# Kernel tuning notes

Hardware: AMD Instinct MI355X
Metric: run time of the kernel (lower is better)

The kernel has to match this reference:

```python
import jax, jax.numpy as jnp
import numpy as np

G, N0, E0 = 10000, 32, 64          # graphs, nodes/graph, edges/graph
NF, NEF, H, D = 64, 64, 128, 256   # num_features, num_edge_features, nhid, ddi_nhid
B = 4096                           # ddi batch_size (pos edges; neg edges follow)
NEG_DECAY = 0.5
RATIO = 0.5


def _lin(k, fan_in, shape):
    s = 1.0 / np.sqrt(fan_in)
    return jax.random.uniform(k, shape, jnp.float32, -s, s)


def setup_inputs() -> dict:
    key = jax.random.key(0)
    ks = jax.random.split(key, 40)
    N, E = G * N0, G * E0
    x = jax.random.normal(ks[0], (N, NF), jnp.float32)
    off = jnp.repeat(jnp.arange(G, dtype=jnp.int32) * N0, E0)
    edge_src = off + jax.random.randint(ks[1], (E,), 0, N0, jnp.int32)
    edge_dst = off + jax.random.randint(ks[2], (E,), 0, N0, jnp.int32)
    edge_weight = jax.random.uniform(ks[3], (E,), jnp.float32)
    ddi_edge_index = jax.random.randint(ks[4], (2, 2 * B), 0, G, jnp.int32)
    ddi_edge_attr = jax.random.normal(ks[5], (2 * B, NEF), jnp.float32)
    p = {}
    p['W1'] = _lin(ks[6], NF, (NF, H)); p['b1'] = jnp.zeros((H,), jnp.float32)
    p['Ws1r'] = _lin(ks[7], H, (H, 1)); p['Ws1n'] = _lin(ks[8], H, (H, 1)); p['bs1'] = jnp.zeros((1,), jnp.float32)
    p['W2'] = _lin(ks[9], H, (H, H)); p['b2'] = jnp.zeros((H,), jnp.float32)
    p['Ws2r'] = _lin(ks[10], H, (H, 1)); p['Ws2n'] = _lin(ks[11], H, (H, 1)); p['bs2'] = jnp.zeros((1,), jnp.float32)
    p['W3'] = _lin(ks[12], H, (H, H)); p['b3'] = jnp.zeros((H,), jnp.float32)
    p['Ws3r'] = _lin(ks[13], H, (H, 1)); p['Ws3n'] = _lin(ks[14], H, (H, 1)); p['bs3'] = jnp.zeros((1,), jnp.float32)
    p['Wd'] = _lin(ks[15], 6 * H, (6 * H, D)); p['bd'] = jnp.zeros((D,), jnp.float32)
    p['Wl1'] = _lin(ks[16], D, (D, D)); p['bl1'] = _lin(ks[17], D, (D,))
    p['Wl2'] = _lin(ks[18], D, (D, D)); p['bl2'] = _lin(ks[19], D, (D,))
    p['Wl3'] = _lin(ks[20], NEF, (NEF, D)); p['bl3'] = _lin(ks[21], NEF, (D,))
    return dict(x=x, edge_src=edge_src, edge_dst=edge_dst, edge_weight=edge_weight,
                ddi_edge_index=ddi_edge_index, ddi_edge_attr=ddi_edge_attr, **p)


def gcn(x, src, dst, ew, W, b):
    # PyG GCNConv: add self-loops (weight 1), symmetric normalization, sum-aggregate
    h = x @ W                                              # [N, out]
    deg = jnp.zeros(x.shape[0], x.dtype).at[dst].add(ew) + 1.0
    dis = jax.lax.rsqrt(deg)
    norm = dis[src] * ew * dis[dst]                        # [E]
    out = jnp.zeros_like(h).at[dst].add(norm[:, None] * h[src])
    out = out + (dis * dis)[:, None] * h                   # self-loop term
    return out + b


def sag_pool(x, src, dst, ew, Wr, Wn, bn, n_per_graph):
    # SAGPooling: score = tanh(GraphConv(x)); keep top ceil(ratio*n) nodes per graph
    N, Hd = x.shape
    g = N // n_per_graph
    agg = jnp.zeros((N, Hd), x.dtype).at[dst].add(ew[:, None] * x[src])
    score = jnp.tanh((agg @ Wn + bn + x @ Wr)[:, 0])       # [N]
    k = int(np.ceil(RATIO * n_per_graph))
    topv, topi = jax.lax.top_k(score.reshape(g, n_per_graph), k)   # [g, k]
    perm = (jnp.arange(g, dtype=jnp.int32)[:, None] * n_per_graph + topi.astype(jnp.int32)).reshape(-1)
    xk = x[perm] * topv.reshape(-1)[:, None]               # gate kept nodes by score
    old2new = jnp.full((N,), -1, jnp.int32).at[perm].set(jnp.arange(g * k, dtype=jnp.int32))
    ns, nd = old2new[src], old2new[dst]
    valid = (ns >= 0) & (nd >= 0)
    new_ew = jnp.where(valid, ew, 0.0)                     # zero-weight == filtered edge
    ns = jnp.where(valid, ns, 0)
    nd = jnp.where(valid, nd, 0)
    return xk, ns, nd, new_ew, k


def readout(x, k):
    # gmp || gap with contiguous, equal-size graphs
    xg = x.reshape(-1, k, x.shape[1])
    return jnp.concatenate([xg.max(axis=1), xg.mean(axis=1)], axis=1)


def reference(x, edge_src, edge_dst, edge_weight, ddi_edge_index, ddi_edge_attr,
              W1, b1, Ws1r, Ws1n, bs1, W2, b2, Ws2r, Ws2n, bs2,
              W3, b3, Ws3r, Ws3n, bs3, Wd, bd, Wl1, bl1, Wl2, bl2, Wl3, bl3):
    h = jax.nn.relu(gcn(x, edge_src, edge_dst, edge_weight, W1, b1))
    h, s, d, ew, k1 = sag_pool(h, edge_src, edge_dst, edge_weight, Ws1r, Ws1n, bs1, N0)
    x1 = readout(h, k1)
    h = jax.nn.relu(gcn(h, s, d, ew, W2, b2))
    h, s, d, ew, k2 = sag_pool(h, s, d, ew, Ws2r, Ws2n, bs2, k1)
    x2 = readout(h, k2)
    h = jax.nn.relu(gcn(h, s, d, ew, W3, b3))
    h, s, d, ew, k3 = sag_pool(h, s, d, ew, Ws3r, Ws3n, bs3, k2)
    x3 = readout(h, k3)
    feat = jnp.concatenate([x1, x2, x3], axis=1)           # [G, 6H] drug features
    # dropout_ratio=0.0 (eval): identity
    ds, dd = ddi_edge_index[0], ddi_edge_index[1]
    dew = jnp.ones(ds.shape, feat.dtype)
    z = jax.nn.relu(gcn(feat, ds, dd, dew, Wd, bd))        # [G, D]
    src_f, tgt_f = z[ds], z[dd]
    pos_x = jax.nn.sigmoid(src_f[:B] @ Wl1 + bl1)
    pos_y = jax.nn.sigmoid(tgt_f[:B] @ Wl2 + bl2)
    neg_x = jax.nn.sigmoid(src_f[B:] @ Wl1 + bl1)
    neg_y = jax.nn.sigmoid(tgt_f[B:] @ Wl2 + bl2)
    pos_a = jax.nn.sigmoid(ddi_edge_attr[:B] @ Wl3 + bl3)
    neg_a = jax.nn.sigmoid(ddi_edge_attr[B:] @ Wl3 + bl3)
    lp = pos_x + pos_a - pos_y
    ln = neg_x + neg_a - neg_y
    norm_pos = jnp.linalg.norm(lp, axis=1)
    norm_neg = jnp.linalg.norm(ln, axis=1)
    loss = 2.0 * D - norm_pos + NEG_DECAY * norm_neg
    return loss, norm_pos, norm_neg, pos_x
```

## Files before the change

### kernel.cpp

```cpp
#include <hip/hip_runtime.h>
#include <math.h>

#define GG   10000
#define NN0  32
#define EE0  64
#define NFF  64
#define HH   128
#define DD   256
#define BB   4096
#define E2B  8192
#define SIXH 768
#define APAD 36

typedef unsigned short u16;
typedef __attribute__((ext_vector_type(8))) short short8v;
typedef __attribute__((ext_vector_type(4))) short short4v;
typedef __attribute__((ext_vector_type(4))) float f32x4;
typedef _Float16 h8f __attribute__((ext_vector_type(8)));
typedef _Float16 h4f __attribute__((ext_vector_type(4)));

static __device__ __forceinline__ u16 f2bf(float x) {
  unsigned u = __float_as_uint(x);
  return (u16)((u + 0x7FFFu + ((u >> 16) & 1u)) >> 16);
}
static __device__ __forceinline__ float bf2f(u16 h) {
  return __uint_as_float(((unsigned)h) << 16);
}


template<int M, int KK, int K, int SX, bool IND, bool LAST>
__device__ __forceinline__ void stage(
    const _Float16* __restrict__ WTh, const _Float16* __restrict__ WTl,
    const float* __restrict__ bg,
    const float* __restrict__ Wr, const float* __restrict__ Wn, const float* __restrict__ bs,
    float* bufX, _Float16* ybh, _Float16* ybl, float* s_A,
    float* s_dis, float* s_cm, float* s_sc2,
    float* s_v1p, float* s_v2p, float* s_score, int* s_rank, int* s_inv,
    int& src_r, int& dst_r, float& ew_r,
    u16* __restrict__ featg, int t)
{
  constexpr int KP = K + 8;
  constexpr int RT  = (M > 16) ? 2 : 1;
  constexpr int CTW = (RT == 2) ? 4 : 2;
  constexpr int KF  = K / 32;
  constexpr int NS  = (RT == 2) ? 2 : 4;

  if (t < EE0)
    atomicAdd(&s_A[dst_r*APAD + src_r], ew_r);
  __syncthreads();

  if (t < M) {
    float deg = 1.f;
#pragma unroll
    for (int m0 = 0; m0 < M; m0 += 4) {
      const float4 a4 = *(const float4*)(s_A + t*APAD + m0);
      deg += a4.x + a4.y + a4.z + a4.w;
    }
    const float dis = rsqrtf(deg);
    const float gg = IND ? s_score[s_inv[t]] : 1.f;
    s_dis[t] = dis; s_cm[t] = dis*gg; s_sc2[t] = dis*dis*gg;
  }
  __syncthreads();

  {
    constexpr int CGB = K/4, RGB = 256/CGB, R = M/RGB;
    const int cg = t % CGB, rg = t / CGB;
    const int c0 = cg * 4;
    float acc[R][4];
#pragma unroll
    for (int i = 0; i < R; ++i) { acc[i][0]=0.f; acc[i][1]=0.f; acc[i][2]=0.f; acc[i][3]=0.f; }
#pragma unroll 2
    for (int m0 = 0; m0 < M; m0 += 4) {
      float4 a[R];
#pragma unroll
      for (int i = 0; i < R; ++i)
        a[i] = *(const float4*)(s_A + (rg*R + i)*APAD + m0);
#pragma unroll
      for (int j = 0; j < 4; ++j) {
        const int m = m0 + j;
        const int row = IND ? s_inv[m] : m;
        const float4 xv = *(const float4*)(bufX + row*SX + c0);
        const float cmm = s_cm[m];
#pragma unroll
        for (int i = 0; i < R; ++i) {
          const float aj = (j==0) ? a[i].x : (j==1) ? a[i].y : (j==2) ? a[i].z : a[i].w;
          const float cf = aj * cmm;
          acc[i][0] = fmaf(cf, xv.x, acc[i][0]);
          acc[i][1] = fmaf(cf, xv.y, acc[i][1]);
          acc[i][2] = fmaf(cf, xv.z, acc[i][2]);
          acc[i][3] = fmaf(cf, xv.w, acc[i][3]);
        }
      }
    }
#pragma unroll
    for (int i = 0; i < R; ++i) {
      const int r = rg*R + i;
      const int rr = IND ? s_inv[r] : r;
      const float4 xv = *(const float4*)(bufX + rr*SX + c0);
      const float dr = s_dis[r], sc = s_sc2[r];
      float4 v;
      v.x = fmaf(sc, xv.x, acc[i][0]*dr);
      v.y = fmaf(sc, xv.y, acc[i][1]*dr);
      v.z = fmaf(sc, xv.z, acc[i][2]*dr);
      v.w = fmaf(sc, xv.w, acc[i][3]*dr);
      h4f vh, vl;
      _Float16 h;
      h = (_Float16)v.x; vh[0] = h; vl[0] = (_Float16)((v.x - (float)h) * 2048.f);
      h = (_Float16)v.y; vh[1] = h; vl[1] = (_Float16)((v.y - (float)h) * 2048.f);
      h = (_Float16)v.z; vh[2] = h; vl[2] = (_Float16)((v.z - (float)h) * 2048.f);
      h = (_Float16)v.w; vh[3] = h; vl[3] = (_Float16)((v.w - (float)h) * 2048.f);
      *(h4f*)(ybh + r*KP + c0) = vh;
      *(h4f*)(ybl + r*KP + c0) = vl;
    }
  }
  __syncthreads();

  {
    const int l = t & 63, w = t >> 6;
    const int l15 = l & 15, kb = l >> 4;
    const int rt   = (RT == 2) ? (w >> 1) : 0;
    const int ct0  = (RT == 2) ? ((w & 1) * CTW) : (w * CTW);
    const int slot = (RT == 2) ? (w & 1) : w;

    h8f ah[KF], al[KF];
#pragma unroll
    for (int kf = 0; kf < KF; ++kf) {
      ah[kf] = *(const h8f*)(ybh + (rt*16 + l15)*KP + kf*32 + kb*8);
      al[kf] = *(const h8f*)(ybl + (rt*16 + l15)*KP + kf*32 + kb*8);
    }
    float p1[4] = {0.f,0.f,0.f,0.f}, p2[4] = {0.f,0.f,0.f,0.f};
#pragma unroll
    for (int ci = 0; ci < CTW; ++ci) {
      const int ct = ct0 + ci;
      const int col = ct*16 + l15;
      f32x4 a0 = {0.f,0.f,0.f,0.f}, a1 = {0.f,0.f,0.f,0.f};
#pragma unroll
      for (int kf = 0; kf < KF; ++kf) {
        const h8f bh = *(const h8f*)(WTh + (size_t)col*K + kf*32 + kb*8);
        const h8f bl = *(const h8f*)(WTl + (size_t)col*K + kf*32 + kb*8);
        a0 = __builtin_amdgcn_mfma_f32_16x16x32_f16(ah[kf], bh, a0, 0, 0, 0);
        a1 = __builtin_amdgcn_mfma_f32_16x16x32_f16(ah[kf], bl, a1, 0, 0, 0);
        a1 = __builtin_amdgcn_mfma_f32_16x16x32_f16(al[kf], bh, a1, 0, 0, 0);
      }
      const float bb = bg[col], wnc = Wn[col], wrc = Wr[col];
#pragma unroll
      for (int j = 0; j < 4; ++j) {
        const int row = rt*16 + kb*4 + j;
        const float o = fmaxf(fmaf(a1[j], (1.f/2048.f), a0[j]) + bb, 0.f);
        bufX[row*HH + col] = o;
        p1[j] = fmaf(o, wnc, p1[j]);
        p2[j] = fmaf(o, wrc, p2[j]);
      }
    }
#pragma unroll
    for (int j = 0; j < 4; ++j) {
#pragma unroll
      for (int off = 8; off >= 1; off >>= 1) {
        p1[j] += __shfl_xor(p1[j], off);
        p2[j] += __shfl_xor(p2[j], off);
      }
    }
    if (l15 == 0) {
#pragma unroll
      for (int j = 0; j < 4; ++j) {
        const int row = rt*16 + kb*4 + j;
        s_v1p[slot*32 + row] = p1[j];
        s_v2p[slot*32 + row] = p2[j];
      }
    }
  }
  __syncthreads();

  if (t < 64) {
    if (t < M) {
      float v2t = s_v2p[t] + s_v2p[32 + t];
      if (NS == 4) v2t += s_v2p[64 + t] + s_v2p[96 + t];
      float sc = bs[0] + v2t;
#pragma unroll
      for (int m0 = 0; m0 < M; m0 += 4) {
        const float4 a4 = *(const float4*)(s_A + t*APAD + m0);
        float4 v4 = *(const float4*)(s_v1p + m0);
        const float4 vb = *(const float4*)(s_v1p + 32 + m0);
        v4.x += vb.x; v4.y += vb.y; v4.z += vb.z; v4.w += vb.w;
        if (NS == 4) {
          const float4 vc = *(const float4*)(s_v1p + 64 + m0);
          const float4 vd = *(const float4*)(s_v1p + 96 + m0);
          v4.x += vc.x + vd.x; v4.y += vc.y + vd.y;
          v4.z += vc.z + vd.z; v4.w += vc.w + vd.w;
        }
        sc += a4.x*v4.x + a4.y*v4.y + a4.z*v4.z + a4.w*v4.w;
      }
      s_score[t] = tanhf(sc);
    }
    if (t < M) {
      const float st = s_score[t];
      int r = 0;
      for (int m = 0; m < M; ++m) {
        const float sm = s_score[m];
        r += (sm > st) || (sm == st && m < t);
      }
      s_rank[t] = r;
      if (r < KK) s_inv[r] = t;
    }
    if (!LAST) {
      const int a = s_rank[src_r];
      const int b = s_rank[dst_r];
      const bool val = (a < KK) && (b < KK);
      ew_r  = val ? ew_r : 0.f;
      src_r = val ? a : 0;
      dst_r = val ? b : 0;
    }
  }
  __syncthreads();

  {
    const int f = t & 127, which = t >> 7;
    float r_acc = which ? 0.f : -INFINITY;
#pragma unroll
    for (int r = 0; r < KK; ++r) {
      const int n = s_inv[r];
      const float v = bufX[n*HH + f] * s_score[n];
      r_acc = which ? (r_acc + v) : fmaxf(r_acc, v);
    }
    featg[which*HH + f] = f2bf(which ? r_acc * (1.f/KK) : r_acc);
  }
  if (!LAST) {
    for (int idx = t; idx < NN0*APAD/4; idx += 256) {
      float4 z4; z4.x = 0.f; z4.y = 0.f; z4.z = 0.f; z4.w = 0.f;
      *(float4*)(s_A + idx*4) = z4;
    }
  }
  __syncthreads();
}

__global__ __launch_bounds__(256, 5) void graph_kernel(
    const float* __restrict__ x,
    const int* __restrict__ esrc, const int* __restrict__ edst, const float* __restrict__ ewg,
    const _Float16* __restrict__ WT,
    const float* __restrict__ b1,
    const float* __restrict__ Ws1r, const float* __restrict__ Ws1n, const float* __restrict__ bs1,
    const float* __restrict__ b2,
    const float* __restrict__ Ws2r, const float* __restrict__ Ws2n, const float* __restrict__ bs2,
    const float* __restrict__ b3,
    const float* __restrict__ Ws3r, const float* __restrict__ Ws3n, const float* __restrict__ bs3,
    u16* __restrict__ featB)
{
  __shared__ __align__(16) float bufX[NN0*HH];
  __shared__ __align__(16) _Float16 ybh[2304], ybl[2304];
  __shared__ __align__(16) float s_A[NN0*APAD];
  __shared__ __align__(16) float s_dis[NN0], s_cm[NN0], s_sc2[NN0], s_score[NN0];
  __shared__ __align__(16) float s_v1p[128], s_v2p[128];
  __shared__ __align__(16) int   s_rank[NN0], s_inv[NN0];

  const int t = threadIdx.x;
  const int g = blockIdx.x;

  for (int idx = t; idx < NN0*NFF/4; idx += 256)
    *(float4*)(bufX + idx*4) = *(const float4*)(x + (size_t)g*NN0*NFF + idx*4);
  int src_r, dst_r; float ew_r;
  {
    const int e = g*EE0 + (t & 63);
    src_r = esrc[e] - g*NN0;
    dst_r = edst[e] - g*NN0;
    ew_r  = ewg[e];
  }
  for (int idx = t; idx < NN0*APAD/4; idx += 256) {
    float4 z4; z4.x = 0.f; z4.y = 0.f; z4.z = 0.f; z4.w = 0.f;
    *(float4*)(s_A + idx*4) = z4;
  }
  __syncthreads();

  u16* featg = featB + (size_t)g * SIXH;
  const _Float16* W1h = WT;
  const _Float16* W1l = W1h + 128*64;
  const _Float16* W2h = W1l + 128*64;
  const _Float16* W2l = W2h + 128*128;
  const _Float16* W3h = W2l + 128*128;
  const _Float16* W3l = W3h + 128*128;

  stage<NN0, 16, NFF, NFF, false, false>(W1h, W1l, b1, Ws1r, Ws1n, bs1,
      bufX, ybh, ybl, s_A, s_dis, s_cm, s_sc2, s_v1p, s_v2p, s_score, s_rank, s_inv,
      src_r, dst_r, ew_r, featg, t);
  stage<16, 8, HH, HH, true, false>(W2h, W2l, b2, Ws2r, Ws2n, bs2,
      bufX, ybh, ybl, s_A, s_dis, s_cm, s_sc2, s_v1p, s_v2p, s_score, s_rank, s_inv,
      src_r, dst_r, ew_r, featg + 256, t);
  stage<8, 4, HH, HH, true, true>(W3h, W3l, b3, Ws3r, Ws3n, bs3,
      bufX, ybh, ybl, s_A, s_dis, s_cm, s_sc2, s_v1p, s_v2p, s_score, s_rank, s_inv,
      src_r, dst_r, ew_r, featg + 512, t);
}

__global__ void k_convW123(const float* __restrict__ W1, const float* __restrict__ W2,
                           const float* __restrict__ W3, _Float16* __restrict__ T)
{
  const int c = blockIdx.x;
  const int k = threadIdx.x;
  _Float16* W1h = T;
  _Float16* W1l = W1h + 128*64;
  _Float16* W2h = W1l + 128*64;
  _Float16* W2l = W2h + 128*128;
  _Float16* W3h = W2l + 128*128;
  _Float16* W3l = W3h + 128*128;
  if (k < 64) {
    const float v = W1[(size_t)k*HH + c];
    const _Float16 h = (_Float16)v;
    W1h[c*64 + k] = h;
    W1l[c*64 + k] = (_Float16)((v - (float)h) * 2048.f);
  }
  {
    const float v = W2[(size_t)k*HH + c];
    const _Float16 h = (_Float16)v;
    W2h[c*HH + k] = h;
    W2l[c*HH + k] = (_Float16)((v - (float)h) * 2048.f);
  }
  {
    const float v = W3[(size_t)k*HH + c];
    const _Float16 h = (_Float16)v;
    W3h[c*HH + k] = h;
    W3l[c*HH + k] = (_Float16)((v - (float)h) * 2048.f);
  }
}


__global__ void k_convW(const float* __restrict__ Wd,
                        const float* __restrict__ Wl1, const float* __restrict__ Wl2,
                        u16* __restrict__ WdT, u16* __restrict__ WlT)
{
  const int b = blockIdx.x, t = threadIdx.x;
  if (b < 256) {
#pragma unroll
    for (int i = 0; i < 3; ++i) {
      const int k = i*256 + t;
      WdT[(size_t)b*SIXH + k] = f2bf(Wd[(size_t)k*DD + b]);
    }
  } else {
    const int c = b - 256;
    const float* src = (c < 256) ? Wl1 : Wl2;
    WlT[(size_t)c*DD + t] = f2bf(src[(size_t)t*DD + (c & 255)]);
  }
}

__global__ void k_deg_init(float* __restrict__ degf) {
  int i = blockIdx.x*256 + threadIdx.x;
  if (i < GG) degf[i] = 1.f;
}

__global__ void k_deg_acc(const int* __restrict__ ddi, float* __restrict__ degf) {
  int e = blockIdx.x*256 + threadIdx.x;
  if (e < E2B) atomicAdd(&degf[ddi[E2B + e]], 1.f);
}

__global__ __launch_bounds__(256) void k_ddi_mfma(const u16* __restrict__ featB,
    const u16* __restrict__ WdT, const float* __restrict__ degf,
    const float* __restrict__ bd, float* __restrict__ hdd, float* __restrict__ z)
{
  const int t = threadIdx.x;
  const int l = t & 63, w = t >> 6;
  const int r0 = blockIdx.x * 16;
  const int l15 = l & 15, kb = l >> 4;
  const int c0 = w * 64;
  f32x4 acc[4];
#pragma unroll
  for (int fi = 0; fi < 4; ++fi) { acc[fi][0]=0.f; acc[fi][1]=0.f; acc[fi][2]=0.f; acc[fi][3]=0.f; }
  const u16* aptr = featB + (size_t)(r0 + l15)*SIXH + kb*8;
#pragma unroll 2
  for (int kk = 0; kk < SIXH; kk += 32) {
    const short8v a = *(const short8v*)(aptr + kk);
#pragma unroll
    for (int fi = 0; fi < 4; ++fi) {
      const short8v b = *(const short8v*)(WdT + (size_t)(c0 + fi*16 + l15)*SIXH + kk + kb*8);
      acc[fi] = __builtin_amdgcn_mfma_f32_16x16x32_bf16(a, b, acc[fi], 0, 0, 0);
    }
  }
#pragma unroll
  for (int j = 0; j < 4; ++j) {
    const int gr = r0 + kb*4 + j;
    const float rd = 1.f / degf[gr];
#pragma unroll
    for (int fi = 0; fi < 4; ++fi) {
      const int c = c0 + fi*16 + l15;
      const float v = acc[fi][j];
      hdd[(size_t)gr*DD + c] = v;
      z[(size_t)gr*DD + c] = fmaf(v, rd, bd[c]);
    }
  }
}

__global__ void k_scatter(const int* __restrict__ ddi, const float* __restrict__ degf,
                          const float* __restrict__ hdd, float* __restrict__ z)
{
  const int t = threadIdx.x;
#pragma unroll
  for (int j = 0; j < 4; ++j) {
    const int e = blockIdx.x*4 + j;
    const int s = ddi[e], d = ddi[E2B + e];
    const float nrm = rsqrtf(degf[s]) * rsqrtf(degf[d]);
    atomicAdd(&z[(size_t)d*DD + t], nrm * hdd[(size_t)s*DD + t]);
  }
}

__global__ void k_zsplit(const float* __restrict__ z,
                         u16* __restrict__ zh, u16* __restrict__ zl)
{
  const int i4 = blockIdx.x*256 + threadIdx.x;
  const float4 v = *(const float4*)(z + (size_t)i4*4);
  short4v h, lo;
  {
    const u16 h0 = f2bf(v.x); h[0] = (short)h0; lo[0] = (short)f2bf(v.x - bf2f(h0));
    const u16 h1 = f2bf(v.y); h[1] = (short)h1; lo[1] = (short)f2bf(v.y - bf2f(h1));
    const u16 h2 = f2bf(v.z); h[2] = (short)h2; lo[2] = (short)f2bf(v.z - bf2f(h2));
    const u16 h3 = f2bf(v.w); h[3] = (short)h3; lo[3] = (short)f2bf(v.w - bf2f(h3));
  }
  *(short4v*)(zh + (size_t)i4*4) = h;
  *(short4v*)(zl + (size_t)i4*4) = lo;
}

__global__ __launch_bounds__(256) void k_xy_mfma(const u16* __restrict__ zh,
    const u16* __restrict__ zl, const u16* __restrict__ WlT,
    const float* __restrict__ bl1, const float* __restrict__ bl2,
    float* __restrict__ X, float* __restrict__ Y)
{
  const int t = threadIdx.x;
  const int l = t & 63, w = t >> 6;
  const int r0 = blockIdx.x * 16;
  const int l15 = l & 15, kb = l >> 4;
  const int c0 = w * 128;
  f32x4 acc[8];
#pragma unroll
  for (int fi = 0; fi < 8; ++fi) { acc[fi][0]=0.f; acc[fi][1]=0.f; acc[fi][2]=0.f; acc[fi][3]=0.f; }
  const u16* ah = zh + (size_t)(r0 + l15)*DD + kb*8;
  const u16* al = zl + (size_t)(r0 + l15)*DD + kb*8;
#pragma unroll 1
  for (int kk = 0; kk < DD; kk += 32) {
    const short8v a0 = *(const short8v*)(ah + kk);
    const short8v a1 = *(const short8v*)(al + kk);
#pragma unroll
    for (int fi = 0; fi < 8; ++fi) {
      const short8v b = *(const short8v*)(WlT + (size_t)(c0 + fi*16 + l15)*DD + kk + kb*8);
      acc[fi] = __builtin_amdgcn_mfma_f32_16x16x32_bf16(a0, b, acc[fi], 0, 0, 0);
      acc[fi] = __builtin_amdgcn_mfma_f32_16x16x32_bf16(a1, b, acc[fi], 0, 0, 0);
    }
  }
#pragma unroll
  for (int fi = 0; fi < 8; ++fi) {
    const int cg = c0 + fi*16 + l15;
    float* dst = (cg < 256) ? X : Y;
    const float bias = (cg < 256) ? bl1[cg] : bl2[cg - 256];
    const int c = cg & 255;
#pragma unroll
    for (int j = 0; j < 4; ++j) {
      const int gr = r0 + kb*4 + j;
      dst[(size_t)gr*DD + c] = 1.f / (1.f + expf(-(acc[fi][j] + bias)));
    }
  }
}

__global__ __launch_bounds__(256) void k_edge(const float* __restrict__ X,
    const float* __restrict__ Y, const int* __restrict__ ddi,
    const float* __restrict__ attr,
    const float* __restrict__ Wl3, const float* __restrict__ bl3,
    float* __restrict__ out)
{
  __shared__ __align__(16) float s_a[8*68];
  __shared__ __align__(16) float s_r[8*257];
  const int t = threadIdx.x;
  const int e0 = blockIdx.x * 8;
  for (int idx = t; idx < 8*64; idx += 256) {
    const int r = idx >> 6, k = idx & 63;
    s_a[r*68 + k] = attr[(size_t)(e0 + r)*NFF + k];
  }
  __syncthreads();
  float acc[8];
#pragma unroll
  for (int r = 0; r < 8; ++r) acc[r] = bl3[t];
#pragma unroll 4
  for (int k = 0; k < 64; ++k) {
    const float w = Wl3[(size_t)k*DD + t];
#pragma unroll
    for (int r = 0; r < 8; ++r) acc[r] = fmaf(s_a[r*68 + k], w, acc[r]);
  }
#pragma unroll
  for (int r = 0; r < 8; ++r) {
    const int e = e0 + r;
    const int s = ddi[e], d = ddi[E2B + e];
    const float xv = X[(size_t)s*DD + t];
    const float yv = Y[(size_t)d*DD + t];
    const float av = 1.f / (1.f + expf(-acc[r]));
    const float lp = xv + av - yv;
    s_r[r*257 + t] = lp * lp;
    if (e < BB) out[12288 + (size_t)e*DD + t] = xv;
  }
  __syncthreads();
  {
    const int row = t >> 5, l = t & 31;
    float s = 0.f;
#pragma unroll
    for (int j = 0; j < 8; ++j) s += s_r[row*257 + l + 32*j];
#pragma unroll
    for (int off = 16; off >= 1; off >>= 1) s += __shfl_xor(s, off);
    if (l == 0) {
      const float nrm = sqrtf(s);
      const int e = e0 + row;
      if (e < BB) out[4096 + e] = nrm;
      else        out[8192 + (e - BB)] = nrm;
    }
  }
}

__global__ void k_loss(float* __restrict__ out) {
  int i = blockIdx.x*256 + threadIdx.x;
  if (i < BB) out[i] = 2.f*(float)DD - out[4096 + i] + 0.5f*out[8192 + i];
}


extern "C" void kernel_launch(void* const* d_in, const int* in_sizes, int n_in,
                              void* d_out, int out_size, void* d_ws, size_t ws_size,
                              hipStream_t stream)
{
  const float* x    = (const float*)d_in[0];
  const int*   esrc = (const int*)d_in[1];
  const int*   edst = (const int*)d_in[2];
  const float* ewt  = (const float*)d_in[3];
  const int*   ddi  = (const int*)d_in[4];
  const float* attr = (const float*)d_in[5];
  const float* W1   = (const float*)d_in[6];  const float* b1  = (const float*)d_in[7];
  const float* Ws1r = (const float*)d_in[8];  const float* Ws1n= (const float*)d_in[9];  const float* bs1 = (const float*)d_in[10];
  const float* W2   = (const float*)d_in[11]; const float* b2  = (const float*)d_in[12];
  const float* Ws2r = (const float*)d_in[13]; const float* Ws2n= (const float*)d_in[14]; const float* bs2 = (const float*)d_in[15];
  const float* W3   = (const float*)d_in[16]; const float* b3  = (const float*)d_in[17];
  const float* Ws3r = (const float*)d_in[18]; const float* Ws3n= (const float*)d_in[19]; const float* bs3 = (const float*)d_in[20];
  const float* Wd   = (const float*)d_in[21]; const float* bd  = (const float*)d_in[22];
  const float* Wl1  = (const float*)d_in[23]; const float* bl1 = (const float*)d_in[24];
  const float* Wl2  = (const float*)d_in[25]; const float* bl2 = (const float*)d_in[26];
  const float* Wl3  = (const float*)d_in[27]; const float* bl3 = (const float*)d_in[28];

  float* ws = (float*)d_ws;
  u16*  featB = (u16*)ws;
  float* hdd  = ws + 3840000;
  float* zb   = hdd + (size_t)GG*DD;
  float* degf = zb  + (size_t)GG*DD;
  u16*  zh    = (u16*)(degf + GG);
  u16*  zl    = zh + (size_t)GG*DD;
  u16*  WdT   = zl + (size_t)GG*DD;
  u16*  WlT   = WdT + 256*SIXH;
  _Float16* WgT = (_Float16*)(WlT + 512*DD);
  float* Xb   = ws;
  float* Yb   = hdd;
  float* out  = (float*)d_out;

  k_convW<<<768, 256, 0, stream>>>(Wd, Wl1, Wl2, WdT, WlT);
  k_convW123<<<128, 128, 0, stream>>>(W1, W2, W3, WgT);
  graph_kernel<<<GG, 256, 0, stream>>>(x, esrc, edst, ewt, WgT,
      b1, Ws1r, Ws1n, bs1, b2, Ws2r, Ws2n, bs2, b3, Ws3r, Ws3n, bs3, featB);
  k_deg_init<<<(GG + 255)/256, 256, 0, stream>>>(degf);
  k_deg_acc<<<(E2B + 255)/256, 256, 0, stream>>>(ddi, degf);
  k_ddi_mfma<<<GG/16, 256, 0, stream>>>(featB, WdT, degf, bd, hdd, zb);
  k_scatter<<<E2B/4, 256, 0, stream>>>(ddi, degf, hdd, zb);
  k_zsplit<<<GG*DD/4/256, 256, 0, stream>>>(zb, zh, zl);
  k_xy_mfma<<<GG/16, 256, 0, stream>>>(zh, zl, WlT, bl1, bl2, Xb, Yb);
  k_edge<<<E2B/8, 256, 0, stream>>>(Xb, Yb, ddi, attr, Wl3, bl3, out);
  k_loss<<<(BB + 255)/256, 256, 0, stream>>>(out);
}
```

Measured before the change: 373.3 us.

## Compute normalized adjacency aggregation with split-fp16 MFMA using transposed fp16 features

Replaces the scalar FMA loop that applied the normalized adjacency to node features with a per-stage dense propagation matrix (built in split hi/lo fp16) multiplied by transposed features via MFMA. Features are now stored in shared memory as transposed hi/lo fp16 pairs instead of fp32, and the pooled-node gather is folded into the propagation matrix through rank lookups. The readout now uses only the high fp16 half, which loses some precision. Shared memory layout changes and launch bounds drop from 5 to 4 blocks per CU, which may reduce occupancy.

```diff
diff --git a/kernel.cpp b/kernel.cpp
--- a/kernel.cpp
+++ b/kernel.cpp
@@ -11,6 +11,8 @@
 #define E2B  8192
 #define SIXH 768
 #define APAD 36
+#define XTS  36
+#define BPS  40
 
 typedef unsigned short u16;
 typedef __attribute__((ext_vector_type(8))) short short8v;
@@ -28,22 +30,24 @@
 }
 
 
-template<int M, int KK, int K, int SX, bool IND, bool LAST>
+template<int M, int P, int KK, int K, int KP, bool FIRST, bool LAST>
 __device__ __forceinline__ void stage(
     const _Float16* __restrict__ WTh, const _Float16* __restrict__ WTl,
     const float* __restrict__ bg,
     const float* __restrict__ Wr, const float* __restrict__ Wn, const float* __restrict__ bs,
-    float* bufX, _Float16* ybh, _Float16* ybl, float* s_A,
-    float* s_dis, float* s_cm, float* s_sc2,
-    float* s_v1p, float* s_v2p, float* s_score, int* s_rank, int* s_inv,
+    _Float16* Xth, _Float16* Xtl, _Float16* ybh, _Float16* ybl,
+    _Float16* Bph, _Float16* Bpl, float* s_A,
+    float* s_dis, float* s_score, int* s_rank, int* s_inv,
+    float* s_v1p, float* s_v2p,
     int& src_r, int& dst_r, float& ew_r,
     u16* __restrict__ featg, int t)
 {
-  constexpr int KP = K + 8;
   constexpr int RT  = (M > 16) ? 2 : 1;
   constexpr int CTW = (RT == 2) ? 4 : 2;
   constexpr int KF  = K / 32;
   constexpr int NS  = (RT == 2) ? 2 : 4;
+  const int l = t & 63, w = t >> 6;
+  const int l15 = l & 15, kb = l >> 4;
 
   if (t < EE0)
     atomicAdd(&s_A[dst_r*APAD + src_r], ew_r);
@@ -56,68 +60,73 @@
       const float4 a4 = *(const float4*)(s_A + t*APAD + m0);
       deg += a4.x + a4.y + a4.z + a4.w;
     }
-    const float dis = rsqrtf(deg);
-    const float gg = IND ? s_score[s_inv[t]] : 1.f;
-    s_dis[t] = dis; s_cm[t] = dis*gg; s_sc2[t] = dis*dis*gg;
-  }
-  __syncthreads();
-
-  {
-    constexpr int CGB = K/4, RGB = 256/CGB, R = M/RGB;
-    const int cg = t % CGB, rg = t / CGB;
-    const int c0 = cg * 4;
-    float acc[R][4];
-#pragma unroll
-    for (int i = 0; i < R; ++i) { acc[i][0]=0.f; acc[i][1]=0.f; acc[i][2]=0.f; acc[i][3]=0.f; }
-#pragma unroll 2
-    for (int m0 = 0; m0 < M; m0 += 4) {
-      float4 a[R];
-#pragma unroll
-      for (int i = 0; i < R; ++i)
-        a[i] = *(const float4*)(s_A + (rg*R + i)*APAD + m0);
-#pragma unroll
-      for (int j = 0; j < 4; ++j) {
-        const int m = m0 + j;
-        const int row = IND ? s_inv[m] : m;
-        const float4 xv = *(const float4*)(bufX + row*SX + c0);
-        const float cmm = s_cm[m];
-#pragma unroll
-        for (int i = 0; i < R; ++i) {
-          const float aj = (j==0) ? a[i].x : (j==1) ? a[i].y : (j==2) ? a[i].z : a[i].w;
-          const float cf = aj * cmm;
-          acc[i][0] = fmaf(cf, xv.x, acc[i][0]);
-          acc[i][1] = fmaf(cf, xv.y, acc[i][1]);
-          acc[i][2] = fmaf(cf, xv.z, acc[i][2]);
-          acc[i][3] = fmaf(cf, xv.w, acc[i][3]);
+    s_dis[t] = rsqrtf(deg);
+  }
+  __syncthreads();
+
+  {
+    constexpr int NE = (M*32 + 255) / 256;
+#pragma unroll
+    for (int n = 0; n < NE; ++n) {
+      const int idx = n*256 + t;
+      if (NE*256 == M*32 || idx < M*32) {
+        const int r = idx >> 5, p = idx & 31;
+        float c = 0.f;
+        if (FIRST) {
+          const float dr = s_dis[r];
+          c = dr * s_A[r*APAD + p] * s_dis[p] + ((p == r) ? dr*dr : 0.f);
+        } else if (p < P) {
+          const int rk = s_rank[p];
+          if (rk < M) {
+            const float sc = s_score[p];
+            const float dr = s_dis[r];
+            c = dr * s_A[r*APAD + rk] * s_dis[rk] * sc
+              + ((rk == r) ? dr*dr*sc : 0.f);
+          }
         }
-      }
-    }
-#pragma unroll
-    for (int i = 0; i < R; ++i) {
-      const int r = rg*R + i;
-      const int rr = IND ? s_inv[r] : r;
-      const float4 xv = *(const float4*)(bufX + rr*SX + c0);
-      const float dr = s_dis[r], sc = s_sc2[r];
-      float4 v;
-      v.x = fmaf(sc, xv.x, acc[i][0]*dr);
-      v.y = fmaf(sc, xv.y, acc[i][1]*dr);
-      v.z = fmaf(sc, xv.z, acc[i][2]*dr);
-      v.w = fmaf(sc, xv.w, acc[i][3]*dr);
-      h4f vh, vl;
-      _Float16 h;
-      h = (_Float16)v.x; vh[0] = h; vl[0] = (_Float16)((v.x - (float)h) * 2048.f);
-      h = (_Float16)v.y; vh[1] = h; vl[1] = (_Float16)((v.y - (float)h) * 2048.f);
-      h = (_Float16)v.z; vh[2] = h; vl[2] = (_Float16)((v.z - (float)h) * 2048.f);
-      h = (_Float16)v.w; vh[3] = h; vl[3] = (_Float16)((v.w - (float)h) * 2048.f);
-      *(h4f*)(ybh + r*KP + c0) = vh;
-      *(h4f*)(ybl + r*KP + c0) = vl;
-    }
-  }
-  __syncthreads();
-
-  {
-    const int l = t & 63, w = t >> 6;
-    const int l15 = l & 15, kb = l >> 4;
+        const _Float16 h = (_Float16)c;
+        Bph[r*BPS + p] = h;
+        Bpl[r*BPS + p] = (_Float16)((c - (float)h) * 2048.f);
+      }
+    }
+  }
+  __syncthreads();
+
+#pragma unroll
+  for (int s = 0; s < 2; ++s) {
+    const int it = (RT == 2) ? s : 0;
+    const int jt = (RT == 2) ? w : (2*w + s);
+    const h8f ah = *(const h8f*)(Bph + (it*16 + l15)*BPS + kb*8);
+    const h8f al = *(const h8f*)(Bpl + (it*16 + l15)*BPS + kb*8);
+    const int f = jt*16 + l15;
+    h8f bh, bl;
+    {
+      const h4f x0 = *(const h4f*)(Xth + f*XTS + kb*8);
+      const h4f x1 = *(const h4f*)(Xth + f*XTS + kb*8 + 4);
+      const h4f y0 = *(const h4f*)(Xtl + f*XTS + kb*8);
+      const h4f y1 = *(const h4f*)(Xtl + f*XTS + kb*8 + 4);
+#pragma unroll
+      for (int u = 0; u < 4; ++u) {
+        bh[u] = x0[u]; bh[u+4] = x1[u];
+        bl[u] = y0[u]; bl[u+4] = y1[u];
+      }
+    }
+    f32x4 a0 = {0.f,0.f,0.f,0.f}, a1 = {0.f,0.f,0.f,0.f};
+    a0 = __builtin_amdgcn_mfma_f32_16x16x32_f16(ah, bh, a0, 0, 0, 0);
+    a1 = __builtin_amdgcn_mfma_f32_16x16x32_f16(ah, bl, a1, 0, 0, 0);
+    a1 = __builtin_amdgcn_mfma_f32_16x16x32_f16(al, bh, a1, 0, 0, 0);
+#pragma unroll
+    for (int j = 0; j < 4; ++j) {
+      const int r  = it*16 + kb*4 + j;
+      const float v = fmaf(a1[j], (1.f/2048.f), a0[j]);
+      const _Float16 h = (_Float16)v;
+      ybh[r*KP + f] = h;
+      ybl[r*KP + f] = (_Float16)((v - (float)h) * 2048.f);
+    }
+  }
+  __syncthreads();
+
+  {
     const int rt   = (RT == 2) ? (w >> 1) : 0;
     const int ct0  = (RT == 2) ? ((w & 1) * CTW) : (w * CTW);
     const int slot = (RT == 2) ? (w & 1) : w;
@@ -147,7 +156,9 @@
       for (int j = 0; j < 4; ++j) {
         const int row = rt*16 + kb*4 + j;
         const float o = fmaxf(fmaf(a1[j], (1.f/2048.f), a0[j]) + bb, 0.f);
-        bufX[row*HH + col] = o;
+        const _Float16 h = (_Float16)o;
+        Xth[col*XTS + row] = h;
+        Xtl[col*XTS + row] = (_Float16)((o - (float)h) * 2048.f);
         p1[j] = fmaf(o, wnc, p1[j]);
         p2[j] = fmaf(o, wrc, p2[j]);
       }
@@ -172,8 +183,9 @@
   __syncthreads();
 
   if (t < 64) {
+    float v1t = 0.f, v2t = 0.f;
     if (t < M) {
-      float v2t = s_v2p[t] + s_v2p[32 + t];
+      v2t = s_v2p[t] + s_v2p[32 + t];
       if (NS == 4) v2t += s_v2p[64 + t] + s_v2p[96 + t];
       float sc = bs[0] + v2t;
 #pragma unroll
@@ -219,7 +231,7 @@
 #pragma unroll
     for (int r = 0; r < KK; ++r) {
       const int n = s_inv[r];
-      const float v = bufX[n*HH + f] * s_score[n];
+      const float v = (float)Xth[f*XTS + n] * s_score[n];
       r_acc = which ? (r_acc + v) : fmaxf(r_acc, v);
     }
     featg[which*HH + f] = f2bf(which ? r_acc * (1.f/KK) : r_acc);
@@ -233,7 +245,7 @@
   __syncthreads();
 }
 
-__global__ __launch_bounds__(256, 5) void graph_kernel(
+__global__ __launch_bounds__(256, 4) void graph_kernel(
     const float* __restrict__ x,
     const int* __restrict__ esrc, const int* __restrict__ edst, const float* __restrict__ ewg,
     const _Float16* __restrict__ WT,
@@ -245,18 +257,26 @@
     const float* __restrict__ Ws3r, const float* __restrict__ Ws3n, const float* __restrict__ bs3,
     u16* __restrict__ featB)
 {
-  __shared__ __align__(16) float bufX[NN0*HH];
+  __shared__ __align__(16) _Float16 Xth[128*XTS], Xtl[128*XTS];
   __shared__ __align__(16) _Float16 ybh[2304], ybl[2304];
+  __shared__ __align__(16) _Float16 Bph[32*BPS], Bpl[32*BPS];
   __shared__ __align__(16) float s_A[NN0*APAD];
-  __shared__ __align__(16) float s_dis[NN0], s_cm[NN0], s_sc2[NN0], s_score[NN0];
+  __shared__ __align__(16) float s_dis[NN0], s_score[NN0];
   __shared__ __align__(16) float s_v1p[128], s_v2p[128];
   __shared__ __align__(16) int   s_rank[NN0], s_inv[NN0];
 
   const int t = threadIdx.x;
   const int g = blockIdx.x;
 
-  for (int idx = t; idx < NN0*NFF/4; idx += 256)
-    *(float4*)(bufX + idx*4) = *(const float4*)(x + (size_t)g*NN0*NFF + idx*4);
+#pragma unroll
+  for (int q = 0; q < 8; ++q) {
+    const int idx = q*256 + t;
+    const int p = idx >> 6, f = idx & 63;
+    const float v = x[(size_t)g*(NN0*NFF) + idx];
+    const _Float16 h = (_Float16)v;
+    Xth[f*XTS + p] = h;
+    Xtl[f*XTS + p] = (_Float16)((v - (float)h) * 2048.f);
+  }
   int src_r, dst_r; float ew_r;
   {
     const int e = g*EE0 + (t & 63);
@@ -278,15 +298,15 @@
   const _Float16* W3h = W2l + 128*128;
   const _Float16* W3l = W3h + 128*128;
 
-  stage<NN0, 16, NFF, NFF, false, false>(W1h, W1l, b1, Ws1r, Ws1n, bs1,
-      bufX, ybh, ybl, s_A, s_dis, s_cm, s_sc2, s_v1p, s_v2p, s_score, s_rank, s_inv,
-      src_r, dst_r, ew_r, featg, t);
-  stage<16, 8, HH, HH, true, false>(W2h, W2l, b2, Ws2r, Ws2n, bs2,
-      bufX, ybh, ybl, s_A, s_dis, s_cm, s_sc2, s_v1p, s_v2p, s_score, s_rank, s_inv,
-      src_r, dst_r, ew_r, featg + 256, t);
-  stage<8, 4, HH, HH, true, true>(W3h, W3l, b3, Ws3r, Ws3n, bs3,
-      bufX, ybh, ybl, s_A, s_dis, s_cm, s_sc2, s_v1p, s_v2p, s_score, s_rank, s_inv,
-      src_r, dst_r, ew_r, featg + 512, t);
+  stage<32, 32, 16,  64,  72, true,  false>(W1h, W1l, b1, Ws1r, Ws1n, bs1,
+      Xth, Xtl, ybh, ybl, Bph, Bpl, s_A, s_dis, s_score, s_rank, s_inv,
+      s_v1p, s_v2p, src_r, dst_r, ew_r, featg, t);
+  stage<16, 32,  8, 128, 136, false, false>(W2h, W2l, b2, Ws2r, Ws2n, bs2,
+      Xth, Xtl, ybh, ybl, Bph, Bpl, s_A, s_dis, s_score, s_rank, s_inv,
+      s_v1p, s_v2p, src_r, dst_r, ew_r, featg + 256, t);
+  stage< 8, 16,  4, 128, 136, false, true >(W3h, W3l, b3, Ws3r, Ws3n, bs3,
+      Xth, Xtl, ybh, ybl, Bph, Bpl, s_A, s_dis, s_score, s_rank, s_inv,
+      s_v1p, s_v2p, src_r, dst_r, ew_r, featg + 512, t);
 }
 
 __global__ void k_convW123(const float* __restrict__ W1, const float* __restrict__ W2,
```

New measurement: 379.0 us. Within noise of the previous version (+1.5%).
